# Kernel optimization log

Measured on AMD Instinct MI355X. Metric: run time of the kernel, lower is better.

The kernel has to match this reference:

```python
import jax, jax.numpy as jnp
import numpy as np

E = 512   # embed_size
H = 8     # num_heads
D = E // H
N = 4
T = 2048


def quantize(x, b, e):
    # fake-quant: scale by 2^e, clamp to signed b-bit range, floor, dequant
    s = jnp.exp2(e)
    lo = -jnp.exp2(b - 1.0)
    hi = jnp.exp2(b - 1.0) - 1.0
    return jnp.floor(jnp.clip(x / s, lo, hi)) * s


def setup_inputs() -> dict:
    key = jax.random.key(0)
    ks = jax.random.split(key, 8)
    f = lambda k, shape: jax.random.normal(k, shape, dtype=jnp.float32)
    w = 1.0 / np.sqrt(E)  # ~ torch Linear init scale
    return {
        "values": f(ks[0], (N, T, E)),
        "keys": f(ks[1], (N, T, E)),
        "query": f(ks[2], (N, T, E)),
        "Wq": f(ks[3], (E, E)) * w, "bq": jnp.zeros((E,), jnp.float32),
        "Wk": f(ks[4], (E, E)) * w, "bk": jnp.zeros((E,), jnp.float32),
        "Wv": f(ks[5], (E, E)) * w, "bv": jnp.zeros((E,), jnp.float32),
        "Wo": f(ks[6], (E, E)) * w, "bo": jnp.zeros((E,), jnp.float32),
        "b_param": jnp.float32(8.0),
        "e_param": jnp.float32(0.0),
    }


def reference(values, keys, query, Wq, bq, Wk, bk, Wv, bv, Wo, bo, b_param, e_param):
    n, t, emb = query.shape
    d = emb // H
    # linear projections (torch Linear: x @ W^T + b), split heads -> [N,H,T,D]
    q = (query @ Wq.T + bq).reshape(n, t, H, d).transpose(0, 2, 1, 3)
    k = (keys @ Wk.T + bk).reshape(n, t, H, d).transpose(0, 2, 1, 3)
    v = (values @ Wv.T + bv).reshape(n, t, H, d).transpose(0, 2, 1, 3)
    b = jnp.clip(b_param, 1.0, 8.0)
    q = quantize(q, b, e_param)
    k = quantize(k, b, e_param)
    v = quantize(v, b, e_param)
    # NOTE: source scales by sqrt(embed_size), not sqrt(head_dim)
    energy = jnp.einsum('nhqd,nhkd->nhqk', q, k) / jnp.sqrt(jnp.float32(emb))
    attn = jax.nn.softmax(energy, axis=-1)
    out = jnp.einsum('nhqk,nhkd->nhqd', attn, v)
    out = out.transpose(0, 2, 1, 3).reshape(n, t, emb)
    return out @ Wo.T + bo
```

## Files before the change

### kernel.cpp

```cpp
#include <hip/hip_runtime.h>
#include <hip/hip_bf16.h>
#include <hip/hip_fp16.h>
#include <cstdint>
#include <cstddef>


typedef __attribute__((ext_vector_type(8))) _Float16 f16x8;
typedef __attribute__((ext_vector_type(2))) __fp16 hf16x2;
typedef __attribute__((ext_vector_type(16))) float f32x16;
typedef __attribute__((ext_vector_type(4))) unsigned u32x4;
typedef unsigned short u16;

#define EL  4194304
#define WEL 262144

static __device__ __forceinline__ u16 f2h(float x) {
  _Float16 h = (_Float16)x;
  return __builtin_bit_cast(u16, h);
}
static __device__ __forceinline__ unsigned pkh2(float a, float b) {
  hf16x2 p = __builtin_amdgcn_cvt_pkrtz(a, b);
  return __builtin_bit_cast(unsigned, p);
}
static __device__ __forceinline__ void gl_lds16(const void* g, void* l) {
  __builtin_amdgcn_global_load_lds(
      (__attribute__((address_space(1))) void*)g,
      (__attribute__((address_space(3))) void*)l, 16, 0, 0);
}

struct PrepAllArgs { const float* src[7]; };

__global__ __launch_bounds__(256) void prep_all_kernel(PrepAllArgs a,
                                                       u16* __restrict__ dst)
{
  const int i = blockIdx.x * 256 + threadIdx.x;
  const float* src; int off;
  if (i < 3145728) {
    const int m = i >> 20; off = i & 1048575;
    src = (m == 0) ? a.src[0] : (m == 1) ? a.src[1] : a.src[2];
  } else {
    const int j = i - 3145728; const int w = j >> 16; off = j & 65535;
    src = (w == 0) ? a.src[3] : (w == 1) ? a.src[4]
        : (w == 2) ? a.src[5] : a.src[6];
  }
  const float4 v = ((const float4*)src)[off];
  ushort4 o;
  o.x = f2h(v.x); o.y = f2h(v.y); o.z = f2h(v.z); o.w = f2h(v.w);
  ((ushort4*)dst)[i] = o;
}

struct ProjArgs {
  const u16* X[3]; const u16* W[3]; const float* bias[3];
  u16* dst[3]; int trans[3];
};

__global__ __launch_bounds__(256, 3) void proj_kernel(ProjArgs args,
    const float* __restrict__ bparam, const float* __restrict__ eparam)
{
  __shared__ u16 sm[17408];
  u16* const As = sm;
  u16* const Bs = sm + 8192;

  const int z = blockIdx.z;
  const u16* __restrict__ X = args.X[z];
  const u16* __restrict__ W = args.W[z];
  const float* __restrict__ bias = args.bias[z];
  u16* __restrict__ dst = args.dst[z];
  const int trans = args.trans[z];

  const int tid  = threadIdx.x;
  const int lane = tid & 63;
  const int wave = tid >> 6;
  const int lam  = lane & 31;
  const int hl   = lane >> 5;
  const int wm   = wave & 1;
  const int wn   = wave >> 1;
  const int mbase = blockIdx.x * 128;
  const int nbase = blockIdx.y * 128;

  const int srow = tid >> 3;
  const int sj   = (tid & 7) ^ (srow & 7);
  const u16* gA = X + (size_t)(mbase + srow) * 512 + sj * 8;
  const u16* gB = W + (size_t)(nbase + srow) * 512 + sj * 8;

  int offA[2][4], offB[2][4];
#pragma unroll
  for (int f = 0; f < 2; ++f)
#pragma unroll
    for (int kk = 0; kk < 4; ++kk) {
      const int c = 2 * kk + hl;
      const int m = wm * 64 + f * 32 + lam;
      offA[f][kk] = m * 128 + ((c ^ (m & 7)) * 16);
      const int nn = wn * 64 + f * 32 + lam;
      offB[f][kk] = nn * 128 + ((c ^ (nn & 7)) * 16);
    }

  f32x16 acc[2][2];
#pragma unroll
  for (int a = 0; a < 2; ++a)
#pragma unroll
    for (int b = 0; b < 2; ++b)
#pragma unroll
      for (int i = 0; i < 16; ++i) acc[a][b][i] = 0.f;

  for (int kt = 0; kt < 512; kt += 64) {
    __syncthreads();
#pragma unroll
    for (int t = 0; t < 4; ++t) {
      gl_lds16(gA + kt + t * 32 * 512, (char*)As + tid * 16 + t * 4096);
      gl_lds16(gB + kt + t * 32 * 512, (char*)Bs + tid * 16 + t * 4096);
    }
    __syncthreads();

    f16x8 fA[2][4], fB[2][4];
#pragma unroll
    for (int f = 0; f < 2; ++f)
#pragma unroll
      for (int kk = 0; kk < 4; ++kk) {
        fA[f][kk] = *(const f16x8*)((const char*)As + offA[f][kk]);
        fB[f][kk] = *(const f16x8*)((const char*)Bs + offB[f][kk]);
      }
#pragma unroll
    for (int mf = 0; mf < 2; ++mf)
#pragma unroll
      for (int nf = 0; nf < 2; ++nf)
#pragma unroll
        for (int kk = 0; kk < 4; ++kk)
          acc[mf][nf] = __builtin_amdgcn_mfma_f32_32x32x16_f16(
              fA[mf][kk], fB[nf][kk], acc[mf][nf], 0, 0, 0);
  }

  const float bq   = fminf(fmaxf(bparam[0], 1.0f), 8.0f);
  const float e    = eparam[0];
  const float s    = exp2f(e);
  const float invs = exp2f(-e);
  const float qlo  = -exp2f(bq - 1.0f);
  const float qhi  = exp2f(bq - 1.0f) - 1.0f;
  const int nidx = mbase >> 11;
  const int tb   = mbase & 2047;
  const int hb   = nbase >> 6;

  if (!trans) {
#pragma unroll
    for (int mf = 0; mf < 2; ++mf)
#pragma unroll
      for (int nf = 0; nf < 2; ++nf)
#pragma unroll
        for (int reg = 0; reg < 16; ++reg) {
          int col = wn * 64 + nf * 32 + lam;
          int row = wm * 64 + mf * 32 + (reg & 3) + 8 * (reg >> 2) + 4 * hl;
          float v = acc[mf][nf][reg] + bias[nbase + col];
          float qv = floorf(fminf(fmaxf(v * invs, qlo), qhi)) * s;
          dst[((size_t)(nidx * 8 + hb + (col >> 6)) * 2048 + tb + row) * 64 +
              (col & 63)] = f2h(qv);
        }
  } else {
    __syncthreads();
#pragma unroll
    for (int mf = 0; mf < 2; ++mf)
#pragma unroll
      for (int nf = 0; nf < 2; ++nf)
#pragma unroll
        for (int reg = 0; reg < 16; ++reg) {
          int col = wn * 64 + nf * 32 + lam;
          int row = wm * 64 + mf * 32 + (reg & 3) + 8 * (reg >> 2) + 4 * hl;
          float v = acc[mf][nf][reg] + bias[nbase + col];
          float qv = floorf(fminf(fmaxf(v * invs, qlo), qhi)) * s;
          sm[col * 136 + row] = f2h(qv);
        }
    __syncthreads();
    const int r = tid >> 1, half = tid & 1;
    const u16* sp = sm + r * 136 + half * 64;
    u16* gp = dst + ((size_t)(nidx * 8 + hb + (r >> 6)) * 64 + (r & 63)) * 2048 +
              tb + half * 64;
#pragma unroll
    for (int i = 0; i < 8; ++i)
      *(uint4*)(gp + i * 8) = *(const uint4*)(sp + i * 8);
  }
}

__global__ __launch_bounds__(256, 2) void attn_kernel(
    const u16* __restrict__ qbuf, const u16* __restrict__ kbuf,
    const u16* __restrict__ vtbuf, u16* __restrict__ ctx)
{
  __shared__ u16 sm[35328];
  char* const smc = (char*)sm;

  const int tid  = threadIdx.x;
  const int wave = tid >> 6;
  const int lane = tid & 63;
  const int lam  = lane & 31;
  const int hl   = lane >> 5;
  const int qt = blockIdx.x, hd = blockIdx.y, n = blockIdx.z;
  const int nh = n * 8 + hd;
  const int qbase = qt * 64;

  const u16* Qp = qbuf + ((size_t)nh * 2048 + qbase) * 64;
  const u16* Kp = kbuf + (size_t)nh * 131072;
  const u16* Vp = vtbuf + (size_t)nh * 131072;

  f16x8 qf[2][4];
#pragma unroll
  for (int qb = 0; qb < 2; ++qb)
#pragma unroll
    for (int dk = 0; dk < 4; ++dk)
      qf[qb][dk] = *(const f16x8*)(Qp + (qb * 32 + lam) * 64 + dk * 16 + hl * 8);

  const float sc = (float)(1.4426950408889634 / 22.627416997969522);

  const int r0 = tid >> 3;
  const int j0 = (tid & 7) ^ (r0 & 7);
  const u16* gK0 = Kp + (size_t)r0 * 64 + j0 * 8;
  const u16* gK1 = Kp + (size_t)(r0 + 32) * 64 + j0 * 8;
  const u16* gV0 = Vp + (size_t)r0 * 2048 + j0 * 8;
  const u16* gV1 = Vp + (size_t)(r0 + 32) * 2048 + j0 * 8;

  int offK[2][4], offV[2][4];
#pragma unroll
  for (int kf = 0; kf < 2; ++kf)
#pragma unroll
    for (int dk = 0; dk < 4; ++dk)
      offK[kf][dk] = wave * 8192 + (kf * 32 + lam) * 128 +
                     (((2 * dk + hl) ^ (lam & 7)) * 16);
#pragma unroll
  for (int nf = 0; nf < 2; ++nf)
#pragma unroll
    for (int kk = 0; kk < 4; ++kk)
      offV[nf][kk] = 32768 + wave * 8192 + (nf * 32 + lam) * 128 +
                     (((2 * kk + hl) ^ (lam & 7)) * 16);

  float l_acc[2] = {0.f, 0.f};
  f32x16 O[2][2];
#pragma unroll
  for (int a = 0; a < 2; ++a)
#pragma unroll
    for (int b = 0; b < 2; ++b)
#pragma unroll
      for (int i = 0; i < 16; ++i) O[a][b][i] = 0.f;

  for (int kt = 0; kt < 2048; kt += 256) {
    __syncthreads();
#pragma unroll
    for (int wt = 0; wt < 4; ++wt) {
      const size_t ko = (size_t)(kt + wt * 64) * 64;
      const int    vo = kt + wt * 64;
      gl_lds16(gK0 + ko, smc + wt * 8192 + tid * 16);
      gl_lds16(gK1 + ko, smc + wt * 8192 + tid * 16 + 4096);
      gl_lds16(gV0 + vo, smc + 32768 + wt * 8192 + tid * 16);
      gl_lds16(gV1 + vo, smc + 32768 + wt * 8192 + tid * 16 + 4096);
    }
    __syncthreads();

#pragma unroll
    for (int kf = 0; kf < 2; ++kf) {
      f16x8 Kf[4], Vf[2][2];
#pragma unroll
      for (int dk = 0; dk < 4; ++dk)
        Kf[dk] = *(const f16x8*)(smc + offK[kf][dk]);
#pragma unroll
      for (int nf = 0; nf < 2; ++nf)
#pragma unroll
        for (int kkl = 0; kkl < 2; ++kkl)
          Vf[nf][kkl] = *(const f16x8*)(smc + offV[nf][2 * kf + kkl]);

#pragma unroll
      for (int qb = 0; qb < 2; ++qb) {
        f32x16 S;
#pragma unroll
        for (int i = 0; i < 16; ++i) S[i] = 0.f;
#pragma unroll
        for (int dk = 0; dk < 4; ++dk)
          S = __builtin_amdgcn_mfma_f32_32x32x16_f16(Kf[dk], qf[qb][dk],
                                                     S, 0, 0, 0);
        unsigned pk[4][2];
#pragma unroll
        for (int gh = 0; gh < 4; ++gh) {
          float p0 = __builtin_amdgcn_exp2f(S[4 * gh + 0] * sc);
          float p1 = __builtin_amdgcn_exp2f(S[4 * gh + 1] * sc);
          float p2 = __builtin_amdgcn_exp2f(S[4 * gh + 2] * sc);
          float p3 = __builtin_amdgcn_exp2f(S[4 * gh + 3] * sc);
          l_acc[qb] += (p0 + p1) + (p2 + p3);
          pk[gh][0] = pkh2(p0, p1);
          pk[gh][1] = pkh2(p2, p3);
        }
        f16x8 pfrag[2];
#pragma unroll
        for (int kkl = 0; kkl < 2; ++kkl) {
          unsigned s0 = hl ? pk[2 * kkl][0] : pk[2 * kkl + 1][0];
          unsigned s1 = hl ? pk[2 * kkl][1] : pk[2 * kkl + 1][1];
          unsigned o0 = hl ? pk[2 * kkl + 1][0] : pk[2 * kkl][0];
          unsigned o1 = hl ? pk[2 * kkl + 1][1] : pk[2 * kkl][1];
          unsigned rr0 = (unsigned)__shfl_xor((int)s0, 32);
          unsigned rr1 = (unsigned)__shfl_xor((int)s1, 32);
          u32x4 f;
          f[0] = hl ? rr0 : o0;
          f[1] = hl ? rr1 : o1;
          f[2] = hl ? o0 : rr0;
          f[3] = hl ? o1 : rr1;
          pfrag[kkl] = __builtin_bit_cast(f16x8, f);
        }
#pragma unroll
        for (int nf = 0; nf < 2; ++nf)
#pragma unroll
          for (int kkl = 0; kkl < 2; ++kkl)
            O[qb][nf] = __builtin_amdgcn_mfma_f32_32x32x16_f16(
                pfrag[kkl], Vf[nf][kkl], O[qb][nf], 0, 0, 0);
      }
    }
  }

#pragma unroll
  for (int qb = 0; qb < 2; ++qb) l_acc[qb] += __shfl_xor(l_acc[qb], 32);
  __syncthreads();
  float* lred = (float*)(smc + 69632);
  if (hl == 0) {
    lred[wave * 64 + lam]      = l_acc[0];
    lred[wave * 64 + 32 + lam] = l_acc[1];
  }
  float* Ow = (float*)(smc + wave * 17408);
#pragma unroll
  for (int qb = 0; qb < 2; ++qb)
#pragma unroll
    for (int nf = 0; nf < 2; ++nf)
#pragma unroll
      for (int r = 0; r < 16; ++r) {
        int qrow = qb * 32 + (r & 3) + 8 * (r >> 2) + 4 * hl;
        Ow[qrow * 68 + nf * 32 + lam] = O[qb][nf][r];
      }
  __syncthreads();

  const int q  = tid >> 2;
  const int d4 = (tid & 3) * 64;
  float acc[16];
  {
    const float4 v0 = *(const float4*)(smc + q * 272 + d4);
    const float4 v1 = *(const float4*)(smc + q * 272 + d4 + 16);
    const float4 v2 = *(const float4*)(smc + q * 272 + d4 + 32);
    const float4 v3 = *(const float4*)(smc + q * 272 + d4 + 48);
    acc[0]=v0.x; acc[1]=v0.y; acc[2]=v0.z; acc[3]=v0.w;
    acc[4]=v1.x; acc[5]=v1.y; acc[6]=v1.z; acc[7]=v1.w;
    acc[8]=v2.x; acc[9]=v2.y; acc[10]=v2.z; acc[11]=v2.w;
    acc[12]=v3.x; acc[13]=v3.y; acc[14]=v3.z; acc[15]=v3.w;
  }
#pragma unroll
  for (int w = 1; w < 4; ++w) {
    const char* b = smc + w * 17408 + q * 272 + d4;
    const float4 v0 = *(const float4*)(b);
    const float4 v1 = *(const float4*)(b + 16);
    const float4 v2 = *(const float4*)(b + 32);
    const float4 v3 = *(const float4*)(b + 48);
    acc[0]+=v0.x; acc[1]+=v0.y; acc[2]+=v0.z; acc[3]+=v0.w;
    acc[4]+=v1.x; acc[5]+=v1.y; acc[6]+=v1.z; acc[7]+=v1.w;
    acc[8]+=v2.x; acc[9]+=v2.y; acc[10]+=v2.z; acc[11]+=v2.w;
    acc[12]+=v3.x; acc[13]+=v3.y; acc[14]+=v3.z; acc[15]+=v3.w;
  }
  const float lsum = lred[q] + lred[64 + q] + lred[128 + q] + lred[192 + q];
  const float rinv = 1.0f / lsum;
  unsigned outp[8];
#pragma unroll
  for (int i = 0; i < 8; ++i)
    outp[i] = pkh2(acc[2 * i] * rinv, acc[2 * i + 1] * rinv);
  u16* cp = ctx + ((size_t)n * 2048 + qbase + q) * 512 + hd * 64 + (tid & 3) * 16;
  *(uint4*)cp       = *(const uint4*)&outp[0];
  *(uint4*)(cp + 8) = *(const uint4*)&outp[4];
}

__global__ __launch_bounds__(256) void outproj_kernel(
    const u16* __restrict__ ctxb, const u16* __restrict__ Wof,
    const float* __restrict__ bias, float* __restrict__ out)
{
  __shared__ u16 sm[12288];
  u16* const As = sm;
  u16* const Bs = sm + 4096;

  const int tid  = threadIdx.x;
  const int lane = tid & 63;
  const int wave = tid >> 6;
  const int lam  = lane & 31;
  const int hl   = lane >> 5;
  const int wm   = wave & 1;
  const int wn   = wave >> 1;
  const int mbase = blockIdx.x * 64;
  const int nbase = blockIdx.y * 128;

  const int srow = tid >> 3;
  const int sj   = (tid & 7) ^ (srow & 7);
  const u16* gA = ctxb + (size_t)(mbase + srow) * 512 + sj * 8;
  const u16* gB = Wof  + (size_t)(nbase + srow) * 512 + sj * 8;

  int offA[4], offB[2][4];
#pragma unroll
  for (int kk = 0; kk < 4; ++kk) {
    const int c = 2 * kk + hl;
    const int m = wm * 32 + lam;
    offA[kk] = m * 128 + ((c ^ (m & 7)) * 16);
#pragma unroll
    for (int f = 0; f < 2; ++f) {
      const int nn = wn * 64 + f * 32 + lam;
      offB[f][kk] = nn * 128 + ((c ^ (nn & 7)) * 16);
    }
  }

  f32x16 acc[2];
#pragma unroll
  for (int a = 0; a < 2; ++a)
#pragma unroll
    for (int i = 0; i < 16; ++i) acc[a][i] = 0.f;

  for (int kt = 0; kt < 512; kt += 64) {
    __syncthreads();
#pragma unroll
    for (int t = 0; t < 2; ++t)
      gl_lds16(gA + kt + t * 32 * 512, (char*)As + tid * 16 + t * 4096);
#pragma unroll
    for (int t = 0; t < 4; ++t)
      gl_lds16(gB + kt + t * 32 * 512, (char*)Bs + tid * 16 + t * 4096);
    __syncthreads();

    f16x8 fA[4], fB[2][4];
#pragma unroll
    for (int kk = 0; kk < 4; ++kk) {
      fA[kk] = *(const f16x8*)((const char*)As + offA[kk]);
#pragma unroll
      for (int f = 0; f < 2; ++f)
        fB[f][kk] = *(const f16x8*)((const char*)Bs + offB[f][kk]);
    }
#pragma unroll
    for (int nf = 0; nf < 2; ++nf)
#pragma unroll
      for (int kk = 0; kk < 4; ++kk)
        acc[nf] = __builtin_amdgcn_mfma_f32_32x32x16_f16(
            fA[kk], fB[nf][kk], acc[nf], 0, 0, 0);
  }

#pragma unroll
  for (int nf = 0; nf < 2; ++nf)
#pragma unroll
    for (int reg = 0; reg < 16; ++reg) {
      int col = nbase + wn * 64 + nf * 32 + lam;
      int row = mbase + wm * 32 + (reg & 3) + 8 * (reg >> 2) + 4 * hl;
      out[(size_t)row * 512 + col] = acc[nf][reg] + bias[col];
    }
}

extern "C" void kernel_launch(void* const* d_in, const int* in_sizes, int n_in,
                              void* d_out, int out_size, void* d_ws, size_t ws_size,
                              hipStream_t stream) {
  (void)in_sizes; (void)n_in; (void)out_size; (void)ws_size;
  const float* values = (const float*)d_in[0];
  const float* keys   = (const float*)d_in[1];
  const float* query  = (const float*)d_in[2];
  const float* Wq = (const float*)d_in[3];  const float* bq = (const float*)d_in[4];
  const float* Wk = (const float*)d_in[5];  const float* bk = (const float*)d_in[6];
  const float* Wv = (const float*)d_in[7];  const float* bv = (const float*)d_in[8];
  const float* Wo = (const float*)d_in[9];  const float* bo = (const float*)d_in[10];
  const float* bp = (const float*)d_in[11]; const float* ep = (const float*)d_in[12];

  u16* ws    = (u16*)d_ws;
  u16* qbuf  = ws;
  u16* kbuf  = ws + (size_t)EL;
  u16* vtbuf = ws + (size_t)2 * EL;
  u16* ctx   = ws + (size_t)3 * EL;
  u16* xwf   = ws + (size_t)4 * EL;

  PrepAllArgs pa;
  pa.src[0] = query; pa.src[1] = keys; pa.src[2] = values;
  pa.src[3] = Wq; pa.src[4] = Wk; pa.src[5] = Wv; pa.src[6] = Wo;
  prep_all_kernel<<<13312, 256, 0, stream>>>(pa, xwf);

  const float* Bsrc[3] = {bq, bk, bv};
  u16* Dst[3] = {qbuf, kbuf, vtbuf};
  ProjArgs a;
  for (int m = 0; m < 3; ++m) {
    a.X[m] = xwf + (size_t)m * EL;
    a.W[m] = xwf + (size_t)3 * EL + (size_t)m * WEL;
    a.bias[m] = Bsrc[m]; a.dst[m] = Dst[m]; a.trans[m] = (m == 2);
  }
  proj_kernel<<<dim3(64, 4, 3), 256, 0, stream>>>(a, bp, ep);

  attn_kernel<<<dim3(32, 8, 4), 256, 0, stream>>>(qbuf, kbuf, vtbuf, ctx);
  outproj_kernel<<<dim3(128, 4), 256, 0, stream>>>(
      ctx, xwf + (size_t)3 * EL + (size_t)3 * WEL, bo, (float*)d_out);
}
```

Baseline: 192.9 us.

## Load V fragments directly from global memory and shrink LDS for higher occupancy

The attention kernel stops staging V tiles through shared memory. Each wave now loads its own V^T fragments straight from global memory into registers, which roughly halves the LDS footprint and raises the launch-bounds occupancy target from 2 to 3 blocks per CU. The epilogue's cross-wave reduction is split into two 32-column passes over a smaller padded buffer so it fits the reduced LDS. In exchange, V reads are strided row accesses from global/L2 rather than coalesced LDS fills, and there is more register pressure under the tighter occupancy bound. The 140-byte row stride also makes the float4 LDS reads not 16-byte aligned.

```diff
diff --git a/kernel.cpp b/kernel.cpp
--- a/kernel.cpp
+++ b/kernel.cpp
@@ -179,11 +179,11 @@
   }
 }
 
-__global__ __launch_bounds__(256, 2) void attn_kernel(
+__global__ __launch_bounds__(256, 3) void attn_kernel(
     const u16* __restrict__ qbuf, const u16* __restrict__ kbuf,
     const u16* __restrict__ vtbuf, u16* __restrict__ ctx)
 {
-  __shared__ u16 sm[35328];
+  __shared__ u16 sm[18432];
   char* const smc = (char*)sm;
 
   const int tid  = threadIdx.x;
@@ -212,22 +212,17 @@
   const int j0 = (tid & 7) ^ (r0 & 7);
   const u16* gK0 = Kp + (size_t)r0 * 64 + j0 * 8;
   const u16* gK1 = Kp + (size_t)(r0 + 32) * 64 + j0 * 8;
-  const u16* gV0 = Vp + (size_t)r0 * 2048 + j0 * 8;
-  const u16* gV1 = Vp + (size_t)(r0 + 32) * 2048 + j0 * 8;
-
-  int offK[2][4], offV[2][4];
+
+  int offK[2][4];
 #pragma unroll
   for (int kf = 0; kf < 2; ++kf)
 #pragma unroll
     for (int dk = 0; dk < 4; ++dk)
       offK[kf][dk] = wave * 8192 + (kf * 32 + lam) * 128 +
                      (((2 * dk + hl) ^ (lam & 7)) * 16);
-#pragma unroll
-  for (int nf = 0; nf < 2; ++nf)
-#pragma unroll
-    for (int kk = 0; kk < 4; ++kk)
-      offV[nf][kk] = 32768 + wave * 8192 + (nf * 32 + lam) * 128 +
-                     (((2 * kk + hl) ^ (lam & 7)) * 16);
+
+  const u16* gV0 = Vp + (size_t)lam * 2048 + wave * 64 + hl * 8;
+  const u16* gV1 = Vp + (size_t)(32 + lam) * 2048 + wave * 64 + hl * 8;
 
   float l_acc[2] = {0.f, 0.f};
   f32x16 O[2][2];
@@ -243,25 +238,23 @@
 #pragma unroll
     for (int wt = 0; wt < 4; ++wt) {
       const size_t ko = (size_t)(kt + wt * 64) * 64;
-      const int    vo = kt + wt * 64;
       gl_lds16(gK0 + ko, smc + wt * 8192 + tid * 16);
       gl_lds16(gK1 + ko, smc + wt * 8192 + tid * 16 + 4096);
-      gl_lds16(gV0 + vo, smc + 32768 + wt * 8192 + tid * 16);
-      gl_lds16(gV1 + vo, smc + 32768 + wt * 8192 + tid * 16 + 4096);
+    }
+    f16x8 Vf[2][4];
+#pragma unroll
+    for (int kk = 0; kk < 4; ++kk) {
+      Vf[0][kk] = *(const f16x8*)(gV0 + kt + kk * 16);
+      Vf[1][kk] = *(const f16x8*)(gV1 + kt + kk * 16);
     }
     __syncthreads();
 
 #pragma unroll
     for (int kf = 0; kf < 2; ++kf) {
-      f16x8 Kf[4], Vf[2][2];
+      f16x8 Kf[4];
 #pragma unroll
       for (int dk = 0; dk < 4; ++dk)
         Kf[dk] = *(const f16x8*)(smc + offK[kf][dk]);
-#pragma unroll
-      for (int nf = 0; nf < 2; ++nf)
-#pragma unroll
-        for (int kkl = 0; kkl < 2; ++kkl)
-          Vf[nf][kkl] = *(const f16x8*)(smc + offV[nf][2 * kf + kkl]);
 
 #pragma unroll
       for (int qb = 0; qb < 2; ++qb) {
@@ -304,65 +297,62 @@
 #pragma unroll
           for (int kkl = 0; kkl < 2; ++kkl)
             O[qb][nf] = __builtin_amdgcn_mfma_f32_32x32x16_f16(
-                pfrag[kkl], Vf[nf][kkl], O[qb][nf], 0, 0, 0);
+                pfrag[kkl], Vf[nf][2 * kf + kkl], O[qb][nf], 0, 0, 0);
       }
     }
   }
 
-#pragma unroll
-  for (int qb = 0; qb < 2; ++qb) l_acc[qb] += __shfl_xor(l_acc[qb], 32);
+  l_acc[0] += __shfl_xor(l_acc[0], 32);
+  l_acc[1] += __shfl_xor(l_acc[1], 32);
   __syncthreads();
-  float* lred = (float*)(smc + 69632);
+  float* lred = (float*)(smc + 35840);
   if (hl == 0) {
     lred[wave * 64 + lam]      = l_acc[0];
     lred[wave * 64 + 32 + lam] = l_acc[1];
   }
-  float* Ow = (float*)(smc + wave * 17408);
-#pragma unroll
-  for (int qb = 0; qb < 2; ++qb)
-#pragma unroll
-    for (int nf = 0; nf < 2; ++nf)
+  float* Ow = (float*)(smc + wave * 8960);
+  float rinv = 0.f;
+  const int q  = tid >> 2;
+  const int sg = tid & 3;
+#pragma unroll
+  for (int nf = 0; nf < 2; ++nf) {
+    if (nf) __syncthreads();
+#pragma unroll
+    for (int qb = 0; qb < 2; ++qb)
 #pragma unroll
       for (int r = 0; r < 16; ++r) {
         int qrow = qb * 32 + (r & 3) + 8 * (r >> 2) + 4 * hl;
-        Ow[qrow * 68 + nf * 32 + lam] = O[qb][nf][r];
+        Ow[qrow * 35 + lam] = O[qb][nf][r];
       }
-  __syncthreads();
-
-  const int q  = tid >> 2;
-  const int d4 = (tid & 3) * 64;
-  float acc[16];
-  {
-    const float4 v0 = *(const float4*)(smc + q * 272 + d4);
-    const float4 v1 = *(const float4*)(smc + q * 272 + d4 + 16);
-    const float4 v2 = *(const float4*)(smc + q * 272 + d4 + 32);
-    const float4 v3 = *(const float4*)(smc + q * 272 + d4 + 48);
-    acc[0]=v0.x; acc[1]=v0.y; acc[2]=v0.z; acc[3]=v0.w;
-    acc[4]=v1.x; acc[5]=v1.y; acc[6]=v1.z; acc[7]=v1.w;
-    acc[8]=v2.x; acc[9]=v2.y; acc[10]=v2.z; acc[11]=v2.w;
-    acc[12]=v3.x; acc[13]=v3.y; acc[14]=v3.z; acc[15]=v3.w;
-  }
-#pragma unroll
-  for (int w = 1; w < 4; ++w) {
-    const char* b = smc + w * 17408 + q * 272 + d4;
-    const float4 v0 = *(const float4*)(b);
-    const float4 v1 = *(const float4*)(b + 16);
-    const float4 v2 = *(const float4*)(b + 32);
-    const float4 v3 = *(const float4*)(b + 48);
-    acc[0]+=v0.x; acc[1]+=v0.y; acc[2]+=v0.z; acc[3]+=v0.w;
-    acc[4]+=v1.x; acc[5]+=v1.y; acc[6]+=v1.z; acc[7]+=v1.w;
-    acc[8]+=v2.x; acc[9]+=v2.y; acc[10]+=v2.z; acc[11]+=v2.w;
-    acc[12]+=v3.x; acc[13]+=v3.y; acc[14]+=v3.z; acc[15]+=v3.w;
-  }
-  const float lsum = lred[q] + lred[64 + q] + lred[128 + q] + lred[192 + q];
-  const float rinv = 1.0f / lsum;
-  unsigned outp[8];
-#pragma unroll
-  for (int i = 0; i < 8; ++i)
-    outp[i] = pkh2(acc[2 * i] * rinv, acc[2 * i + 1] * rinv);
-  u16* cp = ctx + ((size_t)n * 2048 + qbase + q) * 512 + hd * 64 + (tid & 3) * 16;
-  *(uint4*)cp       = *(const uint4*)&outp[0];
-  *(uint4*)(cp + 8) = *(const uint4*)&outp[4];
+    __syncthreads();
+    if (nf == 0) {
+      const float lsum = lred[q] + lred[64 + q] + lred[128 + q] + lred[192 + q];
+      rinv = 1.0f / lsum;
+    }
+    float acc[8];
+    {
+      const char* b0 = smc + q * 140 + sg * 32;
+      const float4 v0 = *(const float4*)(b0);
+      const float4 v1 = *(const float4*)(b0 + 16);
+      acc[0]=v0.x; acc[1]=v0.y; acc[2]=v0.z; acc[3]=v0.w;
+      acc[4]=v1.x; acc[5]=v1.y; acc[6]=v1.z; acc[7]=v1.w;
+    }
+#pragma unroll
+    for (int w = 1; w < 4; ++w) {
+      const char* b = smc + w * 8960 + q * 140 + sg * 32;
+      const float4 v0 = *(const float4*)(b);
+      const float4 v1 = *(const float4*)(b + 16);
+      acc[0]+=v0.x; acc[1]+=v0.y; acc[2]+=v0.z; acc[3]+=v0.w;
+      acc[4]+=v1.x; acc[5]+=v1.y; acc[6]+=v1.z; acc[7]+=v1.w;
+    }
+    unsigned outp[4];
+#pragma unroll
+    for (int i = 0; i < 4; ++i)
+      outp[i] = pkh2(acc[2 * i] * rinv, acc[2 * i + 1] * rinv);
+    u16* cp = ctx + ((size_t)n * 2048 + qbase + q) * 512 + hd * 64 +
+              nf * 32 + sg * 8;
+    *(uint4*)cp = *(const uint4*)&outp[0];
+  }
 }
 
 __global__ __launch_bounds__(256) void outproj_kernel(
```

Measured after the change: 291.3 us. 51.0% more time.
